# Performance work log

Measured on AMD Instinct MI355X. Metric: run time of the kernel, lower is better.

The kernel has to match this reference:

```python
import jax, jax.numpy as jnp
import numpy as np

S, B, D, H = 2048, 4, 1024, 16
HD = D // H  # 64
NEG = -1e9


def _rope_cache(seq_len, dim, base=10000.0):
    inv_freq = 1.0 / (base ** (jnp.arange(0, dim, 2, dtype=jnp.float32) / dim))
    pos = jnp.arange(seq_len, dtype=jnp.float32)
    freqs = jnp.einsum('i,j->ij', pos, inv_freq)          # [S, dim/2]
    emb = jnp.concatenate([freqs, freqs], axis=-1)         # [S, dim]
    return jnp.cos(emb)[None, None], jnp.sin(emb)[None, None]  # [1,1,S,dim]


def _apply_rotary(x, cos, sin):
    # rotated[..., ::2] = -x[..., 1::2]; rotated[..., 1::2] = x[..., ::2]
    x_even = x[..., ::2]
    x_odd = x[..., 1::2]
    rotated = jnp.stack([-x_odd, x_even], axis=-1).reshape(x.shape)
    return x * cos + rotated * sin


def setup_inputs() -> dict:
    key = jax.random.key(0)
    kx, kq, ko = jax.random.split(key, 3)
    x = jax.random.normal(kx, (S, B, D), dtype=jnp.float32)
    # additive causal mask, broadcastable over [B,H,S,S]
    causal = jnp.triu(jnp.full((S, S), NEG, dtype=jnp.float32), k=1)
    cos, sin = _rope_cache(S, HD)
    Wqkv = jax.random.normal(kq, (D, 3 * D), dtype=jnp.float32) * (D ** -0.5)
    Wout = jax.random.normal(ko, (D, D), dtype=jnp.float32) * (D ** -0.5)
    return {"x": x, "attn_mask": causal, "cos": cos, "sin": sin,
            "Wqkv": Wqkv, "Wout": Wout}


def reference(x, attn_mask, cos, sin, Wqkv, Wout):
    scale = 1.0 / jnp.sqrt(jnp.float32(HD))
    xb = jnp.swapaxes(x, 0, 1)                       # [B,S,D]
    qkv = jnp.einsum('bsd,de->bse', xb, Wqkv)        # [B,S,3D]
    q, k, v = jnp.split(qkv, 3, axis=-1)
    def heads(t):
        return t.reshape(B, S, H, HD).transpose(0, 2, 1, 3)  # [B,H,S,HD]
    q, k, v = heads(q), heads(k), heads(v)
    q = _apply_rotary(q, cos, sin)
    k = _apply_rotary(k, cos, sin)
    scores = jnp.einsum('bhsd,bhtd->bhst', q, k) * scale + attn_mask
    probs = jax.nn.softmax(scores, axis=-1)
    ctx = jnp.einsum('bhst,bhtd->bhsd', probs, v)
    ctx = ctx.transpose(0, 2, 1, 3).reshape(B, S, D)  # [B,S,D]
    out = jnp.einsum('bsd,de->bse', ctx, Wout)
    return jnp.swapaxes(out, 0, 1)                    # [S,B,D]
```

## Files before the change

### kernel.cpp

```cpp
#include <hip/hip_runtime.h>
#include <hip/hip_bf16.h>

#define S_LEN 2048
#define BATCH 4
#define DMODEL 1024
#define NHEAD 16
#define HDIM 64
#define E3 3072

typedef __bf16 bf16x8 __attribute__((ext_vector_type(8)));
typedef float f32x4 __attribute__((ext_vector_type(4)));

typedef const __attribute__((address_space(1))) void gvoid;
typedef __attribute__((address_space(3))) void lvoid;

__global__ void cast_f32_bf16(const float* __restrict__ src, __bf16* __restrict__ dst) {
    int i = (blockIdx.x * 256 + threadIdx.x) * 8;
    float4 a = *(const float4*)(src + i);
    float4 b = *(const float4*)(src + i + 4);
    bf16x8 v;
    v[0] = (__bf16)a.x; v[1] = (__bf16)a.y; v[2] = (__bf16)a.z; v[3] = (__bf16)a.w;
    v[4] = (__bf16)b.x; v[5] = (__bf16)b.y; v[6] = (__bf16)b.z; v[7] = (__bf16)b.w;
    *(bf16x8*)(dst + i) = v;
}

__global__ void transpose_f32_bf16(const float* __restrict__ src, __bf16* __restrict__ dst,
                                   int R, int C) {
    __shared__ float tile[32][33];
    int c0 = blockIdx.x * 32, r0 = blockIdx.y * 32;
    int tx = threadIdx.x, ty = threadIdx.y;
#pragma unroll
    for (int i = 0; i < 32; i += 8)
        tile[ty + i][tx] = src[(size_t)(r0 + ty + i) * C + c0 + tx];
    __syncthreads();
#pragma unroll
    for (int i = 0; i < 32; i += 8)
        dst[(size_t)(c0 + ty + i) * R + r0 + tx] = (__bf16)tile[tx][ty + i];
}

__global__ void transpose_v(const __bf16* __restrict__ qkv, __bf16* __restrict__ vt) {
    __shared__ unsigned short tile[64][65];
    int bh = blockIdx.y;
    int s0 = blockIdx.x * 64;
    int tx = threadIdx.x & 31, ty = threadIdx.x >> 5;
    const __bf16* src = qkv + (size_t)(bh >> 4) * S_LEN * E3 + 2 * DMODEL + (bh & 15) * HDIM;
#pragma unroll
    for (int i = 0; i < 8; i++) {
        ushort2 v = *(const ushort2*)(src + (size_t)(s0 + ty + i * 8) * E3 + 2 * tx);
        tile[2 * tx][ty + i * 8] = v.x;
        tile[2 * tx + 1][ty + i * 8] = v.y;
    }
    __syncthreads();
    __bf16* dst = vt + (size_t)bh * HDIM * S_LEN + s0;
#pragma unroll
    for (int i = 0; i < 8; i++) {
        ushort2 v;
        v.x = tile[ty + i * 8][2 * tx];
        v.y = tile[ty + i * 8][2 * tx + 1];
        *(ushort2*)(dst + (size_t)(ty + i * 8) * S_LEN + 2 * tx) = v;
    }
}

__global__ __launch_bounds__(256) void gemm_bt(
    const __bf16* __restrict__ A, const __bf16* __restrict__ BT, void* __restrict__ C,
    int K, int aSB, int aSS, int cSB, int cSS, int cF32) {
    __shared__ __bf16 lA[128 * 32];
    __shared__ __bf16 lB[128 * 32];

    const int tid = threadIdx.x;
    const int lane = tid & 63;
    const int quad = lane >> 4, l16 = lane & 15;
    const int wave = tid >> 6;
    const int wm = wave >> 1, wn = wave & 1;

    const int bid0 = blockIdx.y * gridDim.x + blockIdx.x;
    const int nwg = gridDim.x * gridDim.y;
    const int lid = (bid0 & 7) * (nwg >> 3) + (bid0 >> 3);
    const int bx = lid % gridDim.x;
    const int by = lid / gridDim.x;

    const int rm0 = by * 128;
    const int n0 = bx * 128;
    const int bb = rm0 / S_LEN;
    const int s0 = rm0 % S_LEN;

    const int lrow = lane >> 2;
    const int lch = (lane & 3) * 8;
    const int row0 = wave * 32;
    const __bf16* gA0 = A + (size_t)bb * aSB + (size_t)(s0 + row0 + lrow) * aSS + lch;
    const __bf16* gA1 = A + (size_t)bb * aSB + (size_t)(s0 + row0 + 16 + lrow) * aSS + lch;
    const __bf16* gB0 = BT + (size_t)(n0 + row0 + lrow) * K + lch;
    const __bf16* gB1 = BT + (size_t)(n0 + row0 + 16 + lrow) * K + lch;
    __bf16* ldsA0 = &lA[row0 * 32];
    __bf16* ldsA1 = &lA[(row0 + 16) * 32];
    __bf16* ldsB0 = &lB[row0 * 32];
    __bf16* ldsB1 = &lB[(row0 + 16) * 32];

    f32x4 acc[4][4];
#pragma unroll
    for (int i = 0; i < 4; i++)
#pragma unroll
        for (int j = 0; j < 4; j++) acc[i][j] = (f32x4){0.f, 0.f, 0.f, 0.f};

    for (int k0 = 0; k0 < K; k0 += 32) {
        __builtin_amdgcn_global_load_lds((gvoid*)(gA0 + k0), (lvoid*)ldsA0, 16, 0, 0);
        __builtin_amdgcn_global_load_lds((gvoid*)(gA1 + k0), (lvoid*)ldsA1, 16, 0, 0);
        __builtin_amdgcn_global_load_lds((gvoid*)(gB0 + k0), (lvoid*)ldsB0, 16, 0, 0);
        __builtin_amdgcn_global_load_lds((gvoid*)(gB1 + k0), (lvoid*)ldsB1, 16, 0, 0);
        __syncthreads();

        bf16x8 aF[4], bF[4];
#pragma unroll
        for (int i = 0; i < 4; i++) {
            aF[i] = *(const bf16x8*)&lA[(wm * 64 + i * 16 + l16) * 32 + quad * 8];
            bF[i] = *(const bf16x8*)&lB[(wn * 64 + i * 16 + l16) * 32 + quad * 8];
        }
#pragma unroll
        for (int i = 0; i < 4; i++)
#pragma unroll
            for (int j = 0; j < 4; j++)
                acc[i][j] = __builtin_amdgcn_mfma_f32_16x16x32_bf16(aF[i], bF[j], acc[i][j], 0, 0, 0);
        __syncthreads();
    }

#pragma unroll
    for (int i = 0; i < 4; i++) {
        const int rl = wm * 64 + i * 16 + quad * 4;
#pragma unroll
        for (int r = 0; r < 4; r++) {
            const size_t rowOff = (size_t)bb * cSB + (size_t)(s0 + rl + r) * cSS + n0 + wn * 64 + l16;
            if (cF32) {
                float* cRow = (float*)C + rowOff;
#pragma unroll
                for (int j = 0; j < 4; j++) cRow[j * 16] = acc[i][j][r];
            } else {
                __bf16* cRow = (__bf16*)C + rowOff;
#pragma unroll
                for (int j = 0; j < 4; j++) cRow[j * 16] = (__bf16)acc[i][j][r];
            }
        }
    }
}

__global__ void rope_kernel(__bf16* __restrict__ qkv, const float* __restrict__ cosb,
                            const float* __restrict__ sinb) {
    int idx = blockIdx.x * 256 + threadIdx.x;
    int t8 = idx & 7;
    int h = (idx >> 3) & 15;
    int part = (idx >> 7) & 1;
    int row = idx >> 8;
    int s = row & (S_LEN - 1);
    size_t base = (size_t)row * E3 + part * DMODEL + h * HDIM + t8 * 8;
    bf16x8 v = *(const bf16x8*)(qkv + base);
    const float* cp = cosb + s * HDIM + t8 * 8;
    const float* sp = sinb + s * HDIM + t8 * 8;
    float4 c0 = *(const float4*)cp;
    float4 c1 = *(const float4*)(cp + 4);
    float4 s0 = *(const float4*)sp;
    float4 s1 = *(const float4*)(sp + 4);
    bf16x8 o;
    float x0, x1;
    x0 = (float)v[0]; x1 = (float)v[1];
    o[0] = (__bf16)(x0 * c0.x - x1 * s0.x);
    o[1] = (__bf16)(x1 * c0.y + x0 * s0.y);
    x0 = (float)v[2]; x1 = (float)v[3];
    o[2] = (__bf16)(x0 * c0.z - x1 * s0.z);
    o[3] = (__bf16)(x1 * c0.w + x0 * s0.w);
    x0 = (float)v[4]; x1 = (float)v[5];
    o[4] = (__bf16)(x0 * c1.x - x1 * s1.x);
    o[5] = (__bf16)(x1 * c1.y + x0 * s1.y);
    x0 = (float)v[6]; x1 = (float)v[7];
    o[6] = (__bf16)(x0 * c1.z - x1 * s1.z);
    o[7] = (__bf16)(x1 * c1.w + x0 * s1.w);
    *(bf16x8*)(qkv + base) = o;
}

#define VT_IDX(hd, t) ((hd) * 72 + ((hd) >> 4) * 8 + (t))

__global__ __launch_bounds__(256) void attn_kernel(const __bf16* __restrict__ qkv,
                                                   const __bf16* __restrict__ vt,
                                                   __bf16* __restrict__ ctx) {
    __shared__ __bf16 sK[2][64 * 72];
    __shared__ __bf16 sVT[2][64 * 72 + 32];
    __shared__ __bf16 sP[4 * 2 * 16 * 72];

    const int tid = threadIdx.x, lane = tid & 63, wave = tid >> 6;
    const int quad = lane >> 4, l16 = lane & 15;

    const int bid0 = blockIdx.y * 16 + blockIdx.x;
    const int lid = (bid0 & 7) * 128 + (bid0 >> 3);
    const int pair = lid & 15;
    const int bh = lid >> 4;
    const int b = bh >> 4, h = bh & 15;

    const int qtA = pair, qtB = 31 - pair;
    const int s0A = qtA * 64 + wave * 16;
    const int s0B = qtB * 64 + wave * 16;
    __bf16* PwA = &sP[wave * 2 * 16 * 72];
    __bf16* PwB = PwA + 16 * 72;

    const int srow = tid >> 2;
    const int c0 = (tid & 3) * 16;

    const float qscale = 0.125f * 1.44269504f;
    const __bf16* kBase = qkv + (size_t)(b * S_LEN + srow) * E3 + DMODEL + h * HDIM + c0;
    const __bf16* vBase = vt + ((size_t)bh * HDIM + srow) * S_LEN + c0;

    const __bf16* qbA = qkv + (size_t)(b * S_LEN + s0A) * E3 + h * HDIM + (size_t)l16 * E3;
    const __bf16* qbB = qkv + (size_t)(b * S_LEN + s0B) * E3 + h * HDIM + (size_t)l16 * E3;
    bf16x8 qfA0 = *(const bf16x8*)(qbA + quad * 8);
    bf16x8 qfA1 = *(const bf16x8*)(qbA + 32 + quad * 8);
    bf16x8 qfB0 = *(const bf16x8*)(qbB + quad * 8);
    bf16x8 qfB1 = *(const bf16x8*)(qbB + 32 + quad * 8);
#pragma unroll
    for (int i = 0; i < 8; i++) {
        qfA0[i] = (__bf16)((float)qfA0[i] * qscale);
        qfA1[i] = (__bf16)((float)qfA1[i] * qscale);
        qfB0[i] = (__bf16)((float)qfB0[i] * qscale);
        qfB1[i] = (__bf16)((float)qfB1[i] * qscale);
    }

    f32x4 oA[4], oB[4], lacA, lacB;
#pragma unroll
    for (int j = 0; j < 4; j++) {
        oA[j] = (f32x4){0.f, 0.f, 0.f, 0.f};
        oB[j] = (f32x4){0.f, 0.f, 0.f, 0.f};
    }
    lacA = (f32x4){0.f, 0.f, 0.f, 0.f};
    lacB = (f32x4){0.f, 0.f, 0.f, 0.f};

    bf16x8 ones;
#pragma unroll
    for (int i = 0; i < 8; i++) ones[i] = (__bf16)1.0f;

    const __bf16* kRow = kBase;
    const __bf16* vRow = vBase;
    bf16x8 k0 = *(const bf16x8*)kRow;
    bf16x8 k1 = *(const bf16x8*)(kRow + 8);
    bf16x8 v0 = *(const bf16x8*)vRow;
    bf16x8 v1 = *(const bf16x8*)(vRow + 8);

    const int nT = qtB + 1;
#pragma unroll 1
    for (int it = 0; it < nT; ++it) {
        const int t0 = it * 64;
        __bf16* sKc = sK[it & 1];
        __bf16* sVc = sVT[it & 1];
        *(bf16x8*)&sKc[srow * 72 + c0] = k0;
        *(bf16x8*)&sKc[srow * 72 + c0 + 8] = k1;
        *(bf16x8*)&sVc[VT_IDX(srow, c0)] = v0;
        *(bf16x8*)&sVc[VT_IDX(srow, c0 + 8)] = v1;
        __syncthreads();

        if (it + 1 < nT) {
            kRow += (size_t)64 * E3;
            vRow += 64;
            k0 = *(const bf16x8*)kRow;
            k1 = *(const bf16x8*)(kRow + 8);
            v0 = *(const bf16x8*)vRow;
            v1 = *(const bf16x8*)(vRow + 8);
        }

        const bool aAct = (it <= qtA);

        f32x4 scA[4], scB[4];
        __builtin_amdgcn_s_setprio(1);
#pragma unroll
        for (int j = 0; j < 4; j++) {
            bf16x8 kf0 = *(const bf16x8*)&sKc[(j * 16 + l16) * 72 + quad * 8];
            bf16x8 kf1 = *(const bf16x8*)&sKc[(j * 16 + l16) * 72 + 32 + quad * 8];
            f32x4 z = (f32x4){0.f, 0.f, 0.f, 0.f};
            z = __builtin_amdgcn_mfma_f32_16x16x32_bf16(qfB0, kf0, z, 0, 0, 0);
            scB[j] = __builtin_amdgcn_mfma_f32_16x16x32_bf16(qfB1, kf1, z, 0, 0, 0);
            if (aAct) {
                f32x4 za = (f32x4){0.f, 0.f, 0.f, 0.f};
                za = __builtin_amdgcn_mfma_f32_16x16x32_bf16(qfA0, kf0, za, 0, 0, 0);
                scA[j] = __builtin_amdgcn_mfma_f32_16x16x32_bf16(qfA1, kf1, za, 0, 0, 0);
            }
        }
        __builtin_amdgcn_s_setprio(0);

        if (it == qtB) {
#pragma unroll
            for (int j = 0; j < 4; j++)
#pragma unroll
                for (int r = 0; r < 4; r++) {
                    int sq = s0B + quad * 4 + r, st = t0 + j * 16 + l16;
                    float val = (st > sq) ? -1e9f : scB[j][r];
                    PwB[(quad * 4 + r) * 72 + j * 16 + l16] = (__bf16)__builtin_exp2f(val);
                }
        } else {
#pragma unroll
            for (int j = 0; j < 4; j++)
#pragma unroll
                for (int r = 0; r < 4; r++)
                    PwB[(quad * 4 + r) * 72 + j * 16 + l16] = (__bf16)__builtin_exp2f(scB[j][r]);
        }
        if (aAct) {
            if (it == qtA) {
#pragma unroll
                for (int j = 0; j < 4; j++)
#pragma unroll
                    for (int r = 0; r < 4; r++) {
                        int sq = s0A + quad * 4 + r, st = t0 + j * 16 + l16;
                        float val = (st > sq) ? -1e9f : scA[j][r];
                        PwA[(quad * 4 + r) * 72 + j * 16 + l16] = (__bf16)__builtin_exp2f(val);
                    }
            } else {
#pragma unroll
                for (int j = 0; j < 4; j++)
#pragma unroll
                    for (int r = 0; r < 4; r++)
                        PwA[(quad * 4 + r) * 72 + j * 16 + l16] = (__bf16)__builtin_exp2f(scA[j][r]);
            }
        }

        __builtin_amdgcn_s_setprio(1);
#pragma unroll
        for (int kt = 0; kt < 2; kt++) {
            bf16x8 pfB = *(const bf16x8*)&PwB[l16 * 72 + kt * 32 + quad * 8];
            bf16x8 pfA = pfB;
            if (aAct) pfA = *(const bf16x8*)&PwA[l16 * 72 + kt * 32 + quad * 8];
#pragma unroll
            for (int j = 0; j < 4; j++) {
                bf16x8 vf = *(const bf16x8*)&sVc[VT_IDX(j * 16 + l16, kt * 32 + quad * 8)];
                oB[j] = __builtin_amdgcn_mfma_f32_16x16x32_bf16(pfB, vf, oB[j], 0, 0, 0);
                if (aAct) oA[j] = __builtin_amdgcn_mfma_f32_16x16x32_bf16(pfA, vf, oA[j], 0, 0, 0);
            }
            lacB = __builtin_amdgcn_mfma_f32_16x16x32_bf16(pfB, ones, lacB, 0, 0, 0);
            if (aAct) lacA = __builtin_amdgcn_mfma_f32_16x16x32_bf16(pfA, ones, lacA, 0, 0, 0);
        }
        __builtin_amdgcn_s_setprio(0);
    }

#pragma unroll
    for (int r = 0; r < 4; r++) {
        float inv = 1.f / lacA[r];
        size_t crow = (size_t)(b * S_LEN + s0A + quad * 4 + r) * DMODEL + h * HDIM + l16;
#pragma unroll
        for (int j = 0; j < 4; j++) ctx[crow + j * 16] = (__bf16)(oA[j][r] * inv);
    }
#pragma unroll
    for (int r = 0; r < 4; r++) {
        float inv = 1.f / lacB[r];
        size_t crow = (size_t)(b * S_LEN + s0B + quad * 4 + r) * DMODEL + h * HDIM + l16;
#pragma unroll
        for (int j = 0; j < 4; j++) ctx[crow + j * 16] = (__bf16)(oB[j][r] * inv);
    }
}

extern "C" void kernel_launch(void* const* d_in, const int* in_sizes, int n_in,
                              void* d_out, int out_size, void* d_ws, size_t ws_size,
                              hipStream_t stream) {
    const float* x = (const float*)d_in[0];
    const float* cosb = (const float*)d_in[2];
    const float* sinb = (const float*)d_in[3];
    const float* Wqkv = (const float*)d_in[4];
    const float* Wout = (const float*)d_in[5];
    float* out = (float*)d_out;

    char* ws = (char*)d_ws;
    __bf16* qkv = (__bf16*)ws;
    __bf16* ctx = (__bf16*)(ws + 50331648);
    __bf16* WqkvT = (__bf16*)(ws + 50331648 + 16777216);
    __bf16* WoutT = (__bf16*)(ws + 50331648 + 16777216 + 6291456);
    __bf16* xb = ctx;
    __bf16* vtg = (__bf16*)d_out;

    cast_f32_bf16<<<(S_LEN * BATCH * DMODEL / 8) / 256, 256, 0, stream>>>(x, xb);
    transpose_f32_bf16<<<dim3(E3 / 32, DMODEL / 32), dim3(32, 8), 0, stream>>>(Wqkv, WqkvT, DMODEL, E3);
    transpose_f32_bf16<<<dim3(DMODEL / 32, DMODEL / 32), dim3(32, 8), 0, stream>>>(Wout, WoutT, DMODEL, DMODEL);

    gemm_bt<<<dim3(E3 / 128, (BATCH * S_LEN) / 128), 256, 0, stream>>>(
        xb, WqkvT, qkv, DMODEL,
        DMODEL, BATCH * DMODEL,
        S_LEN * E3, E3, 0);

    transpose_v<<<dim3(S_LEN / 64, BATCH * NHEAD), 256, 0, stream>>>(qkv, vtg);

    rope_kernel<<<(BATCH * S_LEN * 2 * DMODEL / 8) / 256, 256, 0, stream>>>(qkv, cosb, sinb);

    attn_kernel<<<dim3(16, BATCH * NHEAD), 256, 0, stream>>>(qkv, vtg, ctx);

    gemm_bt<<<dim3(DMODEL / 128, (BATCH * S_LEN) / 128), 256, 0, stream>>>(
        ctx, WoutT, out, DMODEL,
        S_LEN * DMODEL, DMODEL,
        DMODEL, BATCH * DMODEL, 1);
}
```

Measured before the change: 337.6 us.

## Enlarge attention query tiles to 128 rows, halving blocks and reusing K/V

Each attention block now handles two 128-row query tiles, with 32 rows per wave and two MFMA row fragments, instead of two 64-row tiles. Each K/V tile loaded into shared memory is therefore reused across twice as many query rows, cutting global K/V traffic and per-tile barriers. The A and B tiles are now processed one after another through a single shared P buffer rather than interleaved. The trade-off is half as many blocks (512), more registers per wave (launch bounds now request one block per SM), and less interleaving of MFMA and exp work, which may lower occupancy and latency hiding.

```diff
diff --git a/kernel.cpp b/kernel.cpp
--- a/kernel.cpp
+++ b/kernel.cpp
@@ -177,27 +177,26 @@
 
 #define VT_IDX(hd, t) ((hd) * 72 + ((hd) >> 4) * 8 + (t))
 
-__global__ __launch_bounds__(256) void attn_kernel(const __bf16* __restrict__ qkv,
-                                                   const __bf16* __restrict__ vt,
-                                                   __bf16* __restrict__ ctx) {
+__global__ __launch_bounds__(256, 1) void attn_kernel(const __bf16* __restrict__ qkv,
+                                                      const __bf16* __restrict__ vt,
+                                                      __bf16* __restrict__ ctx) {
     __shared__ __bf16 sK[2][64 * 72];
     __shared__ __bf16 sVT[2][64 * 72 + 32];
-    __shared__ __bf16 sP[4 * 2 * 16 * 72];
+    __shared__ __bf16 sP[4 * 32 * 72];
 
     const int tid = threadIdx.x, lane = tid & 63, wave = tid >> 6;
     const int quad = lane >> 4, l16 = lane & 15;
 
-    const int bid0 = blockIdx.y * 16 + blockIdx.x;
-    const int lid = (bid0 & 7) * 128 + (bid0 >> 3);
-    const int pair = lid & 15;
-    const int bh = lid >> 4;
+    const int bid0 = blockIdx.y * 8 + blockIdx.x;
+    const int lid = (bid0 & 7) * 64 + (bid0 >> 3);
+    const int pair = lid & 7;
+    const int bh = lid >> 3;
     const int b = bh >> 4, h = bh & 15;
 
-    const int qtA = pair, qtB = 31 - pair;
-    const int s0A = qtA * 64 + wave * 16;
-    const int s0B = qtB * 64 + wave * 16;
-    __bf16* PwA = &sP[wave * 2 * 16 * 72];
-    __bf16* PwB = PwA + 16 * 72;
+    const int qtA = pair, qtB = 15 - pair;
+    const int s0A = qtA * 128 + wave * 32;
+    const int s0B = qtB * 128 + wave * 32;
+    __bf16* Pw = &sP[wave * 32 * 72];
 
     const int srow = tid >> 2;
     const int c0 = (tid & 3) * 16;
@@ -206,28 +205,37 @@
     const __bf16* kBase = qkv + (size_t)(b * S_LEN + srow) * E3 + DMODEL + h * HDIM + c0;
     const __bf16* vBase = vt + ((size_t)bh * HDIM + srow) * S_LEN + c0;
 
-    const __bf16* qbA = qkv + (size_t)(b * S_LEN + s0A) * E3 + h * HDIM + (size_t)l16 * E3;
-    const __bf16* qbB = qkv + (size_t)(b * S_LEN + s0B) * E3 + h * HDIM + (size_t)l16 * E3;
-    bf16x8 qfA0 = *(const bf16x8*)(qbA + quad * 8);
-    bf16x8 qfA1 = *(const bf16x8*)(qbA + 32 + quad * 8);
-    bf16x8 qfB0 = *(const bf16x8*)(qbB + quad * 8);
-    bf16x8 qfB1 = *(const bf16x8*)(qbB + 32 + quad * 8);
-#pragma unroll
-    for (int i = 0; i < 8; i++) {
-        qfA0[i] = (__bf16)((float)qfA0[i] * qscale);
-        qfA1[i] = (__bf16)((float)qfA1[i] * qscale);
-        qfB0[i] = (__bf16)((float)qfB0[i] * qscale);
-        qfB1[i] = (__bf16)((float)qfB1[i] * qscale);
-    }
-
-    f32x4 oA[4], oB[4], lacA, lacB;
-#pragma unroll
-    for (int j = 0; j < 4; j++) {
-        oA[j] = (f32x4){0.f, 0.f, 0.f, 0.f};
-        oB[j] = (f32x4){0.f, 0.f, 0.f, 0.f};
-    }
-    lacA = (f32x4){0.f, 0.f, 0.f, 0.f};
-    lacB = (f32x4){0.f, 0.f, 0.f, 0.f};
+    bf16x8 qfA[2][2], qfB[2][2];
+#pragma unroll
+    for (int mf = 0; mf < 2; mf++) {
+        const __bf16* qa = qkv + (size_t)(b * S_LEN + s0A + mf * 16 + l16) * E3 + h * HDIM;
+        const __bf16* qb = qkv + (size_t)(b * S_LEN + s0B + mf * 16 + l16) * E3 + h * HDIM;
+        qfA[mf][0] = *(const bf16x8*)(qa + quad * 8);
+        qfA[mf][1] = *(const bf16x8*)(qa + 32 + quad * 8);
+        qfB[mf][0] = *(const bf16x8*)(qb + quad * 8);
+        qfB[mf][1] = *(const bf16x8*)(qb + 32 + quad * 8);
+    }
+#pragma unroll
+    for (int mf = 0; mf < 2; mf++)
+#pragma unroll
+        for (int kh = 0; kh < 2; kh++)
+#pragma unroll
+            for (int i = 0; i < 8; i++) {
+                qfA[mf][kh][i] = (__bf16)((float)qfA[mf][kh][i] * qscale);
+                qfB[mf][kh][i] = (__bf16)((float)qfB[mf][kh][i] * qscale);
+            }
+
+    f32x4 oA[2][4], oB[2][4], lacA[2], lacB[2];
+#pragma unroll
+    for (int mf = 0; mf < 2; mf++) {
+#pragma unroll
+        for (int j = 0; j < 4; j++) {
+            oA[mf][j] = (f32x4){0.f, 0.f, 0.f, 0.f};
+            oB[mf][j] = (f32x4){0.f, 0.f, 0.f, 0.f};
+        }
+        lacA[mf] = (f32x4){0.f, 0.f, 0.f, 0.f};
+        lacB[mf] = (f32x4){0.f, 0.f, 0.f, 0.f};
+    }
 
     bf16x8 ones;
 #pragma unroll
@@ -240,7 +248,7 @@
     bf16x8 v0 = *(const bf16x8*)vRow;
     bf16x8 v1 = *(const bf16x8*)(vRow + 8);
 
-    const int nT = qtB + 1;
+    const int nT = 2 * qtB + 2;
 #pragma unroll 1
     for (int it = 0; it < nT; ++it) {
         const int t0 = it * 64;
@@ -261,92 +269,135 @@
             v1 = *(const bf16x8*)(vRow + 8);
         }
 
-        const bool aAct = (it <= qtA);
-
-        f32x4 scA[4], scB[4];
-        __builtin_amdgcn_s_setprio(1);
-#pragma unroll
-        for (int j = 0; j < 4; j++) {
-            bf16x8 kf0 = *(const bf16x8*)&sKc[(j * 16 + l16) * 72 + quad * 8];
-            bf16x8 kf1 = *(const bf16x8*)&sKc[(j * 16 + l16) * 72 + 32 + quad * 8];
-            f32x4 z = (f32x4){0.f, 0.f, 0.f, 0.f};
-            z = __builtin_amdgcn_mfma_f32_16x16x32_bf16(qfB0, kf0, z, 0, 0, 0);
-            scB[j] = __builtin_amdgcn_mfma_f32_16x16x32_bf16(qfB1, kf1, z, 0, 0, 0);
-            if (aAct) {
-                f32x4 za = (f32x4){0.f, 0.f, 0.f, 0.f};
-                za = __builtin_amdgcn_mfma_f32_16x16x32_bf16(qfA0, kf0, za, 0, 0, 0);
-                scA[j] = __builtin_amdgcn_mfma_f32_16x16x32_bf16(qfA1, kf1, za, 0, 0, 0);
-            }
-        }
-        __builtin_amdgcn_s_setprio(0);
-
-        if (it == qtB) {
-#pragma unroll
-            for (int j = 0; j < 4; j++)
-#pragma unroll
-                for (int r = 0; r < 4; r++) {
-                    int sq = s0B + quad * 4 + r, st = t0 + j * 16 + l16;
-                    float val = (st > sq) ? -1e9f : scB[j][r];
-                    PwB[(quad * 4 + r) * 72 + j * 16 + l16] = (__bf16)__builtin_exp2f(val);
+        {
+            f32x4 sc[2][4];
+            __builtin_amdgcn_s_setprio(1);
+#pragma unroll
+            for (int j = 0; j < 4; j++) {
+                bf16x8 kf0 = *(const bf16x8*)&sKc[(j * 16 + l16) * 72 + quad * 8];
+                bf16x8 kf1 = *(const bf16x8*)&sKc[(j * 16 + l16) * 72 + 32 + quad * 8];
+#pragma unroll
+                for (int mf = 0; mf < 2; mf++) {
+                    f32x4 z = (f32x4){0.f, 0.f, 0.f, 0.f};
+                    z = __builtin_amdgcn_mfma_f32_16x16x32_bf16(qfB[mf][0], kf0, z, 0, 0, 0);
+                    sc[mf][j] = __builtin_amdgcn_mfma_f32_16x16x32_bf16(qfB[mf][1], kf1, z, 0, 0, 0);
                 }
-        } else {
-#pragma unroll
-            for (int j = 0; j < 4; j++)
-#pragma unroll
-                for (int r = 0; r < 4; r++)
-                    PwB[(quad * 4 + r) * 72 + j * 16 + l16] = (__bf16)__builtin_exp2f(scB[j][r]);
-        }
-        if (aAct) {
-            if (it == qtA) {
-#pragma unroll
-                for (int j = 0; j < 4; j++)
-#pragma unroll
-                    for (int r = 0; r < 4; r++) {
-                        int sq = s0A + quad * 4 + r, st = t0 + j * 16 + l16;
-                        float val = (st > sq) ? -1e9f : scA[j][r];
-                        PwA[(quad * 4 + r) * 72 + j * 16 + l16] = (__bf16)__builtin_exp2f(val);
-                    }
+            }
+            __builtin_amdgcn_s_setprio(0);
+            if (it >= 2 * qtB) {
+#pragma unroll
+                for (int mf = 0; mf < 2; mf++)
+#pragma unroll
+                    for (int j = 0; j < 4; j++)
+#pragma unroll
+                        for (int r = 0; r < 4; r++) {
+                            int sq = s0B + mf * 16 + quad * 4 + r, st = t0 + j * 16 + l16;
+                            float val = (st > sq) ? -1e9f : sc[mf][j][r];
+                            Pw[(mf * 16 + quad * 4 + r) * 72 + j * 16 + l16] =
+                                (__bf16)__builtin_exp2f(val);
+                        }
             } else {
 #pragma unroll
-                for (int j = 0; j < 4; j++)
-#pragma unroll
-                    for (int r = 0; r < 4; r++)
-                        PwA[(quad * 4 + r) * 72 + j * 16 + l16] = (__bf16)__builtin_exp2f(scA[j][r]);
-            }
-        }
-
-        __builtin_amdgcn_s_setprio(1);
-#pragma unroll
-        for (int kt = 0; kt < 2; kt++) {
-            bf16x8 pfB = *(const bf16x8*)&PwB[l16 * 72 + kt * 32 + quad * 8];
-            bf16x8 pfA = pfB;
-            if (aAct) pfA = *(const bf16x8*)&PwA[l16 * 72 + kt * 32 + quad * 8];
+                for (int mf = 0; mf < 2; mf++)
+#pragma unroll
+                    for (int j = 0; j < 4; j++)
+#pragma unroll
+                        for (int r = 0; r < 4; r++)
+                            Pw[(mf * 16 + quad * 4 + r) * 72 + j * 16 + l16] =
+                                (__bf16)__builtin_exp2f(sc[mf][j][r]);
+            }
+            __builtin_amdgcn_s_setprio(1);
+#pragma unroll
+            for (int kt = 0; kt < 2; kt++) {
+                bf16x8 pf0 = *(const bf16x8*)&Pw[l16 * 72 + kt * 32 + quad * 8];
+                bf16x8 pf1 = *(const bf16x8*)&Pw[(16 + l16) * 72 + kt * 32 + quad * 8];
+#pragma unroll
+                for (int j = 0; j < 4; j++) {
+                    bf16x8 vf = *(const bf16x8*)&sVc[VT_IDX(j * 16 + l16, kt * 32 + quad * 8)];
+                    oB[0][j] = __builtin_amdgcn_mfma_f32_16x16x32_bf16(pf0, vf, oB[0][j], 0, 0, 0);
+                    oB[1][j] = __builtin_amdgcn_mfma_f32_16x16x32_bf16(pf1, vf, oB[1][j], 0, 0, 0);
+                }
+                lacB[0] = __builtin_amdgcn_mfma_f32_16x16x32_bf16(pf0, ones, lacB[0], 0, 0, 0);
+                lacB[1] = __builtin_amdgcn_mfma_f32_16x16x32_bf16(pf1, ones, lacB[1], 0, 0, 0);
+            }
+            __builtin_amdgcn_s_setprio(0);
+        }
+
+        if (it <= 2 * qtA + 1) {
+            f32x4 sc[2][4];
+            __builtin_amdgcn_s_setprio(1);
 #pragma unroll
             for (int j = 0; j < 4; j++) {
-                bf16x8 vf = *(const bf16x8*)&sVc[VT_IDX(j * 16 + l16, kt * 32 + quad * 8)];
-                oB[j] = __builtin_amdgcn_mfma_f32_16x16x32_bf16(pfB, vf, oB[j], 0, 0, 0);
-                if (aAct) oA[j] = __builtin_amdgcn_mfma_f32_16x16x32_bf16(pfA, vf, oA[j], 0, 0, 0);
-            }
-            lacB = __builtin_amdgcn_mfma_f32_16x16x32_bf16(pfB, ones, lacB, 0, 0, 0);
-            if (aAct) lacA = __builtin_amdgcn_mfma_f32_16x16x32_bf16(pfA, ones, lacA, 0, 0, 0);
-        }
-        __builtin_amdgcn_s_setprio(0);
-    }
-
-#pragma unroll
-    for (int r = 0; r < 4; r++) {
-        float inv = 1.f / lacA[r];
-        size_t crow = (size_t)(b * S_LEN + s0A + quad * 4 + r) * DMODEL + h * HDIM + l16;
-#pragma unroll
-        for (int j = 0; j < 4; j++) ctx[crow + j * 16] = (__bf16)(oA[j][r] * inv);
-    }
-#pragma unroll
-    for (int r = 0; r < 4; r++) {
-        float inv = 1.f / lacB[r];
-        size_t crow = (size_t)(b * S_LEN + s0B + quad * 4 + r) * DMODEL + h * HDIM + l16;
-#pragma unroll
-        for (int j = 0; j < 4; j++) ctx[crow + j * 16] = (__bf16)(oB[j][r] * inv);
-    }
+                bf16x8 kf0 = *(const bf16x8*)&sKc[(j * 16 + l16) * 72 + quad * 8];
+                bf16x8 kf1 = *(const bf16x8*)&sKc[(j * 16 + l16) * 72 + 32 + quad * 8];
+#pragma unroll
+                for (int mf = 0; mf < 2; mf++) {
+                    f32x4 z = (f32x4){0.f, 0.f, 0.f, 0.f};
+                    z = __builtin_amdgcn_mfma_f32_16x16x32_bf16(qfA[mf][0], kf0, z, 0, 0, 0);
+                    sc[mf][j] = __builtin_amdgcn_mfma_f32_16x16x32_bf16(qfA[mf][1], kf1, z, 0, 0, 0);
+                }
+            }
+            __builtin_amdgcn_s_setprio(0);
+            if (it >= 2 * qtA) {
+#pragma unroll
+                for (int mf = 0; mf < 2; mf++)
+#pragma unroll
+                    for (int j = 0; j < 4; j++)
+#pragma unroll
+                        for (int r = 0; r < 4; r++) {
+                            int sq = s0A + mf * 16 + quad * 4 + r, st = t0 + j * 16 + l16;
+                            float val = (st > sq) ? -1e9f : sc[mf][j][r];
+                            Pw[(mf * 16 + quad * 4 + r) * 72 + j * 16 + l16] =
+                                (__bf16)__builtin_exp2f(val);
+                        }
+            } else {
+#pragma unroll
+                for (int mf = 0; mf < 2; mf++)
+#pragma unroll
+                    for (int j = 0; j < 4; j++)
+#pragma unroll
+                        for (int r = 0; r < 4; r++)
+                            Pw[(mf * 16 + quad * 4 + r) * 72 + j * 16 + l16] =
+                                (__bf16)__builtin_exp2f(sc[mf][j][r]);
+            }
+            __builtin_amdgcn_s_setprio(1);
+#pragma unroll
+            for (int kt = 0; kt < 2; kt++) {
+                bf16x8 pf0 = *(const bf16x8*)&Pw[l16 * 72 + kt * 32 + quad * 8];
+                bf16x8 pf1 = *(const bf16x8*)&Pw[(16 + l16) * 72 + kt * 32 + quad * 8];
+#pragma unroll
+                for (int j = 0; j < 4; j++) {
+                    bf16x8 vf = *(const bf16x8*)&sVc[VT_IDX(j * 16 + l16, kt * 32 + quad * 8)];
+                    oA[0][j] = __builtin_amdgcn_mfma_f32_16x16x32_bf16(pf0, vf, oA[0][j], 0, 0, 0);
+                    oA[1][j] = __builtin_amdgcn_mfma_f32_16x16x32_bf16(pf1, vf, oA[1][j], 0, 0, 0);
+                }
+                lacA[0] = __builtin_amdgcn_mfma_f32_16x16x32_bf16(pf0, ones, lacA[0], 0, 0, 0);
+                lacA[1] = __builtin_amdgcn_mfma_f32_16x16x32_bf16(pf1, ones, lacA[1], 0, 0, 0);
+            }
+            __builtin_amdgcn_s_setprio(0);
+        }
+    }
+
+#pragma unroll
+    for (int mf = 0; mf < 2; mf++)
+#pragma unroll
+        for (int r = 0; r < 4; r++) {
+            float inv = 1.f / lacA[mf][r];
+            size_t crow =
+                (size_t)(b * S_LEN + s0A + mf * 16 + quad * 4 + r) * DMODEL + h * HDIM + l16;
+#pragma unroll
+            for (int j = 0; j < 4; j++) ctx[crow + j * 16] = (__bf16)(oA[mf][j][r] * inv);
+        }
+#pragma unroll
+    for (int mf = 0; mf < 2; mf++)
+#pragma unroll
+        for (int r = 0; r < 4; r++) {
+            float inv = 1.f / lacB[mf][r];
+            size_t crow =
+                (size_t)(b * S_LEN + s0B + mf * 16 + quad * 4 + r) * DMODEL + h * HDIM + l16;
+#pragma unroll
+            for (int j = 0; j < 4; j++) ctx[crow + j * 16] = (__bf16)(oB[mf][j][r] * inv);
+        }
 }
 
 extern "C" void kernel_launch(void* const* d_in, const int* in_sizes, int n_in,
@@ -380,7 +431,7 @@
 
     rope_kernel<<<(BATCH * S_LEN * 2 * DMODEL / 8) / 256, 256, 0, stream>>>(qkv, cosb, sinb);
 
-    attn_kernel<<<dim3(16, BATCH * NHEAD), 256, 0, stream>>>(qkv, vtg, ctx);
+    attn_kernel<<<dim3(8, BATCH * NHEAD), 256, 0, stream>>>(qkv, vtg, ctx);
 
     gemm_bt<<<dim3(DMODEL / 128, (BATCH * S_LEN) / 128), 256, 0, stream>>>(
         ctx, WoutT, out, DMODEL,
```

Measured after the change: 335.3 us. No clear change (-0.7%).

## Keep attention probabilities in registers via transposed QK^T MFMA, drop LDS P buffer

Applied to the files above, without the earlier changes.

The QK^T MFMA now takes K as the A operand and Q as the B operand, so the output layout places key positions along the per-lane register axis. The exp2 probabilities can then be packed straight into the PV MFMA operand in registers, removing the shared-memory round-trip for P and the sP buffer. V fragments are read as two 4-element LDS loads to match the reordered key index. The A and B query tiles are processed sequentially to cut live registers, and launch bounds request 4 blocks per SM. The risks are narrower LDS reads for V, more register pressure from the occupancy hint, and losing the interleaving between the A and B tile MFMAs.

```diff
diff --git a/kernel.cpp b/kernel.cpp
--- a/kernel.cpp
+++ b/kernel.cpp
@@ -9,6 +9,7 @@
 #define E3 3072
 
 typedef __bf16 bf16x8 __attribute__((ext_vector_type(8)));
+typedef __bf16 bf16x4 __attribute__((ext_vector_type(4)));
 typedef float f32x4 __attribute__((ext_vector_type(4)));
 
 typedef const __attribute__((address_space(1))) void gvoid;
@@ -177,12 +178,11 @@
 
 #define VT_IDX(hd, t) ((hd) * 72 + ((hd) >> 4) * 8 + (t))
 
-__global__ __launch_bounds__(256) void attn_kernel(const __bf16* __restrict__ qkv,
-                                                   const __bf16* __restrict__ vt,
-                                                   __bf16* __restrict__ ctx) {
+__global__ __launch_bounds__(256, 4) void attn_kernel(const __bf16* __restrict__ qkv,
+                                                      const __bf16* __restrict__ vt,
+                                                      __bf16* __restrict__ ctx) {
     __shared__ __bf16 sK[2][64 * 72];
     __shared__ __bf16 sVT[2][64 * 72 + 32];
-    __shared__ __bf16 sP[4 * 2 * 16 * 72];
 
     const int tid = threadIdx.x, lane = tid & 63, wave = tid >> 6;
     const int quad = lane >> 4, l16 = lane & 15;
@@ -196,8 +196,6 @@
     const int qtA = pair, qtB = 31 - pair;
     const int s0A = qtA * 64 + wave * 16;
     const int s0B = qtB * 64 + wave * 16;
-    __bf16* PwA = &sP[wave * 2 * 16 * 72];
-    __bf16* PwB = PwA + 16 * 72;
 
     const int srow = tid >> 2;
     const int c0 = (tid & 3) * 16;
@@ -206,8 +204,8 @@
     const __bf16* kBase = qkv + (size_t)(b * S_LEN + srow) * E3 + DMODEL + h * HDIM + c0;
     const __bf16* vBase = vt + ((size_t)bh * HDIM + srow) * S_LEN + c0;
 
-    const __bf16* qbA = qkv + (size_t)(b * S_LEN + s0A) * E3 + h * HDIM + (size_t)l16 * E3;
-    const __bf16* qbB = qkv + (size_t)(b * S_LEN + s0B) * E3 + h * HDIM + (size_t)l16 * E3;
+    const __bf16* qbA = qkv + (size_t)(b * S_LEN + s0A + l16) * E3 + h * HDIM;
+    const __bf16* qbB = qkv + (size_t)(b * S_LEN + s0B + l16) * E3 + h * HDIM;
     bf16x8 qfA0 = *(const bf16x8*)(qbA + quad * 8);
     bf16x8 qfA1 = *(const bf16x8*)(qbA + 32 + quad * 8);
     bf16x8 qfB0 = *(const bf16x8*)(qbB + quad * 8);
@@ -261,76 +259,107 @@
             v1 = *(const bf16x8*)(vRow + 8);
         }
 
-        const bool aAct = (it <= qtA);
-
-        f32x4 scA[4], scB[4];
-        __builtin_amdgcn_s_setprio(1);
-#pragma unroll
-        for (int j = 0; j < 4; j++) {
-            bf16x8 kf0 = *(const bf16x8*)&sKc[(j * 16 + l16) * 72 + quad * 8];
-            bf16x8 kf1 = *(const bf16x8*)&sKc[(j * 16 + l16) * 72 + 32 + quad * 8];
-            f32x4 z = (f32x4){0.f, 0.f, 0.f, 0.f};
-            z = __builtin_amdgcn_mfma_f32_16x16x32_bf16(qfB0, kf0, z, 0, 0, 0);
-            scB[j] = __builtin_amdgcn_mfma_f32_16x16x32_bf16(qfB1, kf1, z, 0, 0, 0);
-            if (aAct) {
-                f32x4 za = (f32x4){0.f, 0.f, 0.f, 0.f};
-                za = __builtin_amdgcn_mfma_f32_16x16x32_bf16(qfA0, kf0, za, 0, 0, 0);
-                scA[j] = __builtin_amdgcn_mfma_f32_16x16x32_bf16(qfA1, kf1, za, 0, 0, 0);
-            }
-        }
-        __builtin_amdgcn_s_setprio(0);
-
-        if (it == qtB) {
-#pragma unroll
-            for (int j = 0; j < 4; j++)
-#pragma unroll
-                for (int r = 0; r < 4; r++) {
-                    int sq = s0B + quad * 4 + r, st = t0 + j * 16 + l16;
-                    float val = (st > sq) ? -1e9f : scB[j][r];
-                    PwB[(quad * 4 + r) * 72 + j * 16 + l16] = (__bf16)__builtin_exp2f(val);
-                }
-        } else {
-#pragma unroll
-            for (int j = 0; j < 4; j++)
-#pragma unroll
-                for (int r = 0; r < 4; r++)
-                    PwB[(quad * 4 + r) * 72 + j * 16 + l16] = (__bf16)__builtin_exp2f(scB[j][r]);
-        }
-        if (aAct) {
-            if (it == qtA) {
-#pragma unroll
-                for (int j = 0; j < 4; j++)
+        {
+            f32x4 sc[4];
+            __builtin_amdgcn_s_setprio(1);
+#pragma unroll
+            for (int jt = 0; jt < 4; jt++) {
+                bf16x8 kf0 = *(const bf16x8*)&sKc[(jt * 16 + l16) * 72 + quad * 8];
+                bf16x8 kf1 = *(const bf16x8*)&sKc[(jt * 16 + l16) * 72 + 32 + quad * 8];
+                f32x4 z = (f32x4){0.f, 0.f, 0.f, 0.f};
+                z = __builtin_amdgcn_mfma_f32_16x16x32_bf16(kf0, qfB0, z, 0, 0, 0);
+                sc[jt] = __builtin_amdgcn_mfma_f32_16x16x32_bf16(kf1, qfB1, z, 0, 0, 0);
+            }
+            __builtin_amdgcn_s_setprio(0);
+
+            float p[4][4];
+            if (it == qtB) {
+                const int qq = s0B + l16;
+#pragma unroll
+                for (int jt = 0; jt < 4; jt++)
 #pragma unroll
                     for (int r = 0; r < 4; r++) {
-                        int sq = s0A + quad * 4 + r, st = t0 + j * 16 + l16;
-                        float val = (st > sq) ? -1e9f : scA[j][r];
-                        PwA[(quad * 4 + r) * 72 + j * 16 + l16] = (__bf16)__builtin_exp2f(val);
+                        int tt = t0 + jt * 16 + quad * 4 + r;
+                        p[jt][r] = __builtin_exp2f((tt > qq) ? -1e9f : sc[jt][r]);
                     }
             } else {
 #pragma unroll
-                for (int j = 0; j < 4; j++)
-#pragma unroll
-                    for (int r = 0; r < 4; r++)
-                        PwA[(quad * 4 + r) * 72 + j * 16 + l16] = (__bf16)__builtin_exp2f(scA[j][r]);
-            }
+                for (int jt = 0; jt < 4; jt++)
+#pragma unroll
+                    for (int r = 0; r < 4; r++) p[jt][r] = __builtin_exp2f(sc[jt][r]);
+            }
+
+            __builtin_amdgcn_s_setprio(1);
+#pragma unroll
+            for (int kt = 0; kt < 2; kt++) {
+                bf16x8 pf;
+#pragma unroll
+                for (int r = 0; r < 4; r++) {
+                    pf[r] = (__bf16)p[2 * kt][r];
+                    pf[4 + r] = (__bf16)p[2 * kt + 1][r];
+                }
+#pragma unroll
+                for (int jhd = 0; jhd < 4; jhd++) {
+                    bf16x4 vlo = *(const bf16x4*)&sVc[VT_IDX(jhd * 16 + l16, kt * 32 + quad * 4)];
+                    bf16x4 vhi = *(const bf16x4*)&sVc[VT_IDX(jhd * 16 + l16, kt * 32 + 16 + quad * 4)];
+                    bf16x8 vf = __builtin_shufflevector(vlo, vhi, 0, 1, 2, 3, 4, 5, 6, 7);
+                    oB[jhd] = __builtin_amdgcn_mfma_f32_16x16x32_bf16(pf, vf, oB[jhd], 0, 0, 0);
+                }
+                lacB = __builtin_amdgcn_mfma_f32_16x16x32_bf16(pf, ones, lacB, 0, 0, 0);
+            }
+            __builtin_amdgcn_s_setprio(0);
         }
 
-        __builtin_amdgcn_s_setprio(1);
-#pragma unroll
-        for (int kt = 0; kt < 2; kt++) {
-            bf16x8 pfB = *(const bf16x8*)&PwB[l16 * 72 + kt * 32 + quad * 8];
-            bf16x8 pfA = pfB;
-            if (aAct) pfA = *(const bf16x8*)&PwA[l16 * 72 + kt * 32 + quad * 8];
-#pragma unroll
-            for (int j = 0; j < 4; j++) {
-                bf16x8 vf = *(const bf16x8*)&sVc[VT_IDX(j * 16 + l16, kt * 32 + quad * 8)];
-                oB[j] = __builtin_amdgcn_mfma_f32_16x16x32_bf16(pfB, vf, oB[j], 0, 0, 0);
-                if (aAct) oA[j] = __builtin_amdgcn_mfma_f32_16x16x32_bf16(pfA, vf, oA[j], 0, 0, 0);
-            }
-            lacB = __builtin_amdgcn_mfma_f32_16x16x32_bf16(pfB, ones, lacB, 0, 0, 0);
-            if (aAct) lacA = __builtin_amdgcn_mfma_f32_16x16x32_bf16(pfA, ones, lacA, 0, 0, 0);
+        if (it <= qtA) {
+            f32x4 sc[4];
+            __builtin_amdgcn_s_setprio(1);
+#pragma unroll
+            for (int jt = 0; jt < 4; jt++) {
+                bf16x8 kf0 = *(const bf16x8*)&sKc[(jt * 16 + l16) * 72 + quad * 8];
+                bf16x8 kf1 = *(const bf16x8*)&sKc[(jt * 16 + l16) * 72 + 32 + quad * 8];
+                f32x4 z = (f32x4){0.f, 0.f, 0.f, 0.f};
+                z = __builtin_amdgcn_mfma_f32_16x16x32_bf16(kf0, qfA0, z, 0, 0, 0);
+                sc[jt] = __builtin_amdgcn_mfma_f32_16x16x32_bf16(kf1, qfA1, z, 0, 0, 0);
+            }
+            __builtin_amdgcn_s_setprio(0);
+
+            float p[4][4];
+            if (it == qtA) {
+                const int qq = s0A + l16;
+#pragma unroll
+                for (int jt = 0; jt < 4; jt++)
+#pragma unroll
+                    for (int r = 0; r < 4; r++) {
+                        int tt = t0 + jt * 16 + quad * 4 + r;
+                        p[jt][r] = __builtin_exp2f((tt > qq) ? -1e9f : sc[jt][r]);
+                    }
+            } else {
+#pragma unroll
+                for (int jt = 0; jt < 4; jt++)
+#pragma unroll
+                    for (int r = 0; r < 4; r++) p[jt][r] = __builtin_exp2f(sc[jt][r]);
+            }
+
+            __builtin_amdgcn_s_setprio(1);
+#pragma unroll
+            for (int kt = 0; kt < 2; kt++) {
+                bf16x8 pf;
+#pragma unroll
+                for (int r = 0; r < 4; r++) {
+                    pf[r] = (__bf16)p[2 * kt][r];
+                    pf[4 + r] = (__bf16)p[2 * kt + 1][r];
+                }
+#pragma unroll
+                for (int jhd = 0; jhd < 4; jhd++) {
+                    bf16x4 vlo = *(const bf16x4*)&sVc[VT_IDX(jhd * 16 + l16, kt * 32 + quad * 4)];
+                    bf16x4 vhi = *(const bf16x4*)&sVc[VT_IDX(jhd * 16 + l16, kt * 32 + 16 + quad * 4)];
+                    bf16x8 vf = __builtin_shufflevector(vlo, vhi, 0, 1, 2, 3, 4, 5, 6, 7);
+                    oA[jhd] = __builtin_amdgcn_mfma_f32_16x16x32_bf16(pf, vf, oA[jhd], 0, 0, 0);
+                }
+                lacA = __builtin_amdgcn_mfma_f32_16x16x32_bf16(pf, ones, lacA, 0, 0, 0);
+            }
+            __builtin_amdgcn_s_setprio(0);
         }
-        __builtin_amdgcn_s_setprio(0);
     }
 
 #pragma unroll
```

New measurement: 336.8 us. About the same (-0.3%).

## Keep attention probabilities in registers by computing transposed score tiles

Applied to the files above, without the earlier changes.

The QK^T MFMA operands are swapped so each lane holds scores along the key dimension, which lets the exp'd probabilities be packed straight into the PV MFMA A-operand registers. This removes the per-wave shared-memory P buffer and its write/read round trip. The V fragments are now loaded as two 4-element halves so they match the permuted key ordering. This costs a second, narrower LDS read for each V fragment and somewhat more register pressure.

```diff
diff --git a/kernel.cpp b/kernel.cpp
--- a/kernel.cpp
+++ b/kernel.cpp
@@ -9,6 +9,7 @@
 #define E3 3072
 
 typedef __bf16 bf16x8 __attribute__((ext_vector_type(8)));
+typedef __bf16 bf16x4 __attribute__((ext_vector_type(4)));
 typedef float f32x4 __attribute__((ext_vector_type(4)));
 
 typedef const __attribute__((address_space(1))) void gvoid;
@@ -182,7 +183,6 @@
                                                    __bf16* __restrict__ ctx) {
     __shared__ __bf16 sK[2][64 * 72];
     __shared__ __bf16 sVT[2][64 * 72 + 32];
-    __shared__ __bf16 sP[4 * 2 * 16 * 72];
 
     const int tid = threadIdx.x, lane = tid & 63, wave = tid >> 6;
     const int quad = lane >> 4, l16 = lane & 15;
@@ -196,8 +196,6 @@
     const int qtA = pair, qtB = 31 - pair;
     const int s0A = qtA * 64 + wave * 16;
     const int s0B = qtB * 64 + wave * 16;
-    __bf16* PwA = &sP[wave * 2 * 16 * 72];
-    __bf16* PwB = PwA + 16 * 72;
 
     const int srow = tid >> 2;
     const int c0 = (tid & 3) * 16;
@@ -206,8 +204,8 @@
     const __bf16* kBase = qkv + (size_t)(b * S_LEN + srow) * E3 + DMODEL + h * HDIM + c0;
     const __bf16* vBase = vt + ((size_t)bh * HDIM + srow) * S_LEN + c0;
 
-    const __bf16* qbA = qkv + (size_t)(b * S_LEN + s0A) * E3 + h * HDIM + (size_t)l16 * E3;
-    const __bf16* qbB = qkv + (size_t)(b * S_LEN + s0B) * E3 + h * HDIM + (size_t)l16 * E3;
+    const __bf16* qbA = qkv + (size_t)(b * S_LEN + s0A + l16) * E3 + h * HDIM;
+    const __bf16* qbB = qkv + (size_t)(b * S_LEN + s0B + l16) * E3 + h * HDIM;
     bf16x8 qfA0 = *(const bf16x8*)(qbA + quad * 8);
     bf16x8 qfA1 = *(const bf16x8*)(qbA + 32 + quad * 8);
     bf16x8 qfB0 = *(const bf16x8*)(qbB + quad * 8);
@@ -263,72 +261,82 @@
 
         const bool aAct = (it <= qtA);
 
-        f32x4 scA[4], scB[4];
+        f32x4 scB[4], scA[4];
         __builtin_amdgcn_s_setprio(1);
 #pragma unroll
-        for (int j = 0; j < 4; j++) {
-            bf16x8 kf0 = *(const bf16x8*)&sKc[(j * 16 + l16) * 72 + quad * 8];
-            bf16x8 kf1 = *(const bf16x8*)&sKc[(j * 16 + l16) * 72 + 32 + quad * 8];
-            f32x4 z = (f32x4){0.f, 0.f, 0.f, 0.f};
-            z = __builtin_amdgcn_mfma_f32_16x16x32_bf16(qfB0, kf0, z, 0, 0, 0);
-            scB[j] = __builtin_amdgcn_mfma_f32_16x16x32_bf16(qfB1, kf1, z, 0, 0, 0);
+        for (int jt = 0; jt < 4; jt++) {
+            bf16x8 kf0 = *(const bf16x8*)&sKc[(jt * 16 + l16) * 72 + quad * 8];
+            bf16x8 kf1 = *(const bf16x8*)&sKc[(jt * 16 + l16) * 72 + 32 + quad * 8];
+            f32x4 zB = (f32x4){0.f, 0.f, 0.f, 0.f};
+            zB = __builtin_amdgcn_mfma_f32_16x16x32_bf16(kf0, qfB0, zB, 0, 0, 0);
+            scB[jt] = __builtin_amdgcn_mfma_f32_16x16x32_bf16(kf1, qfB1, zB, 0, 0, 0);
             if (aAct) {
-                f32x4 za = (f32x4){0.f, 0.f, 0.f, 0.f};
-                za = __builtin_amdgcn_mfma_f32_16x16x32_bf16(qfA0, kf0, za, 0, 0, 0);
-                scA[j] = __builtin_amdgcn_mfma_f32_16x16x32_bf16(qfA1, kf1, za, 0, 0, 0);
+                f32x4 zA = (f32x4){0.f, 0.f, 0.f, 0.f};
+                zA = __builtin_amdgcn_mfma_f32_16x16x32_bf16(kf0, qfA0, zA, 0, 0, 0);
+                scA[jt] = __builtin_amdgcn_mfma_f32_16x16x32_bf16(kf1, qfA1, zA, 0, 0, 0);
             }
         }
         __builtin_amdgcn_s_setprio(0);
 
+        bf16x8 pfB[2], pfA[2];
         if (it == qtB) {
-#pragma unroll
-            for (int j = 0; j < 4; j++)
+            const int qq = s0B + l16;
+#pragma unroll
+            for (int kt = 0; kt < 2; kt++)
 #pragma unroll
                 for (int r = 0; r < 4; r++) {
-                    int sq = s0B + quad * 4 + r, st = t0 + j * 16 + l16;
-                    float val = (st > sq) ? -1e9f : scB[j][r];
-                    PwB[(quad * 4 + r) * 72 + j * 16 + l16] = (__bf16)__builtin_exp2f(val);
+                    int tt0 = t0 + (2 * kt) * 16 + quad * 4 + r;
+                    int tt1 = t0 + (2 * kt + 1) * 16 + quad * 4 + r;
+                    pfB[kt][r] = (__bf16)__builtin_exp2f((tt0 > qq) ? -1e9f : scB[2 * kt][r]);
+                    pfB[kt][4 + r] = (__bf16)__builtin_exp2f((tt1 > qq) ? -1e9f : scB[2 * kt + 1][r]);
                 }
         } else {
 #pragma unroll
-            for (int j = 0; j < 4; j++)
-#pragma unroll
-                for (int r = 0; r < 4; r++)
-                    PwB[(quad * 4 + r) * 72 + j * 16 + l16] = (__bf16)__builtin_exp2f(scB[j][r]);
+            for (int kt = 0; kt < 2; kt++)
+#pragma unroll
+                for (int r = 0; r < 4; r++) {
+                    pfB[kt][r] = (__bf16)__builtin_exp2f(scB[2 * kt][r]);
+                    pfB[kt][4 + r] = (__bf16)__builtin_exp2f(scB[2 * kt + 1][r]);
+                }
         }
         if (aAct) {
             if (it == qtA) {
-#pragma unroll
-                for (int j = 0; j < 4; j++)
+                const int qq = s0A + l16;
+#pragma unroll
+                for (int kt = 0; kt < 2; kt++)
 #pragma unroll
                     for (int r = 0; r < 4; r++) {
-                        int sq = s0A + quad * 4 + r, st = t0 + j * 16 + l16;
-                        float val = (st > sq) ? -1e9f : scA[j][r];
-                        PwA[(quad * 4 + r) * 72 + j * 16 + l16] = (__bf16)__builtin_exp2f(val);
+                        int tt0 = t0 + (2 * kt) * 16 + quad * 4 + r;
+                        int tt1 = t0 + (2 * kt + 1) * 16 + quad * 4 + r;
+                        pfA[kt][r] = (__bf16)__builtin_exp2f((tt0 > qq) ? -1e9f : scA[2 * kt][r]);
+                        pfA[kt][4 + r] =
+                            (__bf16)__builtin_exp2f((tt1 > qq) ? -1e9f : scA[2 * kt + 1][r]);
                     }
             } else {
 #pragma unroll
-                for (int j = 0; j < 4; j++)
-#pragma unroll
-                    for (int r = 0; r < 4; r++)
-                        PwA[(quad * 4 + r) * 72 + j * 16 + l16] = (__bf16)__builtin_exp2f(scA[j][r]);
+                for (int kt = 0; kt < 2; kt++)
+#pragma unroll
+                    for (int r = 0; r < 4; r++) {
+                        pfA[kt][r] = (__bf16)__builtin_exp2f(scA[2 * kt][r]);
+                        pfA[kt][4 + r] = (__bf16)__builtin_exp2f(scA[2 * kt + 1][r]);
+                    }
             }
         }
 
         __builtin_amdgcn_s_setprio(1);
 #pragma unroll
         for (int kt = 0; kt < 2; kt++) {
-            bf16x8 pfB = *(const bf16x8*)&PwB[l16 * 72 + kt * 32 + quad * 8];
-            bf16x8 pfA = pfB;
-            if (aAct) pfA = *(const bf16x8*)&PwA[l16 * 72 + kt * 32 + quad * 8];
-#pragma unroll
-            for (int j = 0; j < 4; j++) {
-                bf16x8 vf = *(const bf16x8*)&sVc[VT_IDX(j * 16 + l16, kt * 32 + quad * 8)];
-                oB[j] = __builtin_amdgcn_mfma_f32_16x16x32_bf16(pfB, vf, oB[j], 0, 0, 0);
-                if (aAct) oA[j] = __builtin_amdgcn_mfma_f32_16x16x32_bf16(pfA, vf, oA[j], 0, 0, 0);
+#pragma unroll
+            for (int jhd = 0; jhd < 4; jhd++) {
+                bf16x4 vlo = *(const bf16x4*)&sVc[VT_IDX(jhd * 16 + l16, kt * 32 + quad * 4)];
+                bf16x4 vhi = *(const bf16x4*)&sVc[VT_IDX(jhd * 16 + l16, kt * 32 + 16 + quad * 4)];
+                bf16x8 vf = __builtin_shufflevector(vlo, vhi, 0, 1, 2, 3, 4, 5, 6, 7);
+                oB[jhd] = __builtin_amdgcn_mfma_f32_16x16x32_bf16(pfB[kt], vf, oB[jhd], 0, 0, 0);
+                if (aAct)
+                    oA[jhd] = __builtin_amdgcn_mfma_f32_16x16x32_bf16(pfA[kt], vf, oA[jhd], 0, 0, 0);
             }
-            lacB = __builtin_amdgcn_mfma_f32_16x16x32_bf16(pfB, ones, lacB, 0, 0, 0);
-            if (aAct) lacA = __builtin_amdgcn_mfma_f32_16x16x32_bf16(pfA, ones, lacA, 0, 0, 0);
+            lacB = __builtin_amdgcn_mfma_f32_16x16x32_bf16(pfB[kt], ones, lacB, 0, 0, 0);
+            if (aAct) lacA = __builtin_amdgcn_mfma_f32_16x16x32_bf16(pfA[kt], ones, lacA, 0, 0, 0);
         }
         __builtin_amdgcn_s_setprio(0);
     }
```

Measured after the change: 319.3 us. 5.4% less time.
